# Kernel optimization log

Measured on AMD Instinct MI355X. Metric: run time of the kernel, lower is better.

The kernel has to match this reference:

```python
import jax, jax.numpy as jnp
import numpy as np

H = 16            # num_heads
DK = 64           # head_k_dim = hidden*0.5/H
DV = 128          # head_v_dim = hidden*1.0/H
EPS = 1e-5
GATE_NORM = 16.0


def setup_inputs() -> dict:
    key = jax.random.key(0)
    ks = jax.random.split(key, 8)
    B, T, D = 4, 4096, 2048
    hidden_states = jax.random.normal(ks[0], (B, T, D), jnp.float32)
    state = jax.random.normal(ks[1], (B, H, DK, DV), jnp.float32)
    norm_w = jnp.ones((D,), jnp.float32)
    # fan-in scaled init so activations stay O(1)
    k_w = jax.random.normal(ks[2], (H * DK, D), jnp.float32) / np.sqrt(D)
    v_w = jax.random.normal(ks[3], (H * DV, D), jnp.float32) / np.sqrt(D)
    gk_w1 = jax.random.normal(ks[4], (16, D), jnp.float32) / np.sqrt(D)
    gk_w2 = jax.random.normal(ks[5], (H * DK, 16), jnp.float32) / np.sqrt(16)
    gk_b = jnp.zeros((H * DK,), jnp.float32)
    return {"hidden_states": hidden_states, "state": state, "norm_w": norm_w,
            "k_w": k_w, "v_w": v_w, "gk_w1": gk_w1, "gk_w2": gk_w2, "gk_b": gk_b}


def reference(hidden_states, state, norm_w, k_w, v_w, gk_w1, gk_w2, gk_b):
    B, T, D = hidden_states.shape
    # RMSNorm
    x = hidden_states * jax.lax.rsqrt(jnp.mean(hidden_states * hidden_states, -1, keepdims=True) + EPS)
    x = x * norm_w
    # projections -> [B,T,H,d]
    k = (x @ k_w.T).reshape(B, T, H, DK)
    v = (x @ v_w.T).reshape(B, T, H, DV)
    gk = jax.nn.log_sigmoid((x @ gk_w1.T) @ gk_w2.T + gk_b) / GATE_NORM  # <= 0
    gk = gk.reshape(B, T, H, DK)
    # GLA recurrence S_t = diag(exp(gk_t)) S_{t-1} + k_t^T v_t, unrolled:
    # S_T = exp(G_T) * S_0 + sum_t exp(G_T - G_t) * k_t v_t^T, G_t = cumsum(gk)
    G = jnp.cumsum(gk, axis=1)                       # [B,T,H,DK]
    g_total = G[:, -1]                               # [B,H,DK]
    decay = jnp.exp(G[:, -1:, :, :] - G)             # in (0,1], stable
    new_state = jnp.exp(g_total)[..., None] * state + \
        jnp.einsum('bthk,bthv->bhkv', k * decay, v)
    return new_state
```

## Files before the change

### kernel.cpp

```cpp
#include <hip/hip_runtime.h>

#define B_ 4
#define T_ 4096
#define D_ 2048
#define H_ 16
#define DK_ 64
#define DV_ 128
#define HDK 1024
#define HDV 2048
#define NN 3072
#define MM 16384
#define NT_ 32

typedef unsigned short u16;
typedef unsigned int u32;
typedef __attribute__((ext_vector_type(8))) short bf16x8;
typedef __attribute__((ext_vector_type(4))) float f32x4;

typedef const __attribute__((address_space(1))) u16 gu16;
typedef __attribute__((address_space(3))) u16 lu16;

__device__ __forceinline__ float b2f(u16 u) {
  u32 x = ((u32)u) << 16; float f; __builtin_memcpy(&f, &x, 4); return f;
}
__device__ __forceinline__ u16 f2b(float f) {
  u32 x; __builtin_memcpy(&x, &f, 4);
  u32 r = x + 0x7FFFu + ((x >> 16) & 1u);
  return (u16)(r >> 16);
}
__device__ __forceinline__ float fexp(float x) { return exp2f(x * 1.44269504f); }
__device__ __forceinline__ float flogsig(float z) {
  float u = exp2f(-fabsf(z) * 1.44269504f);
  float l = log2f(1.f + u) * 0.69314718f;
  return fminf(z, 0.f) - l;
}

__global__ __launch_bounds__(256) void k_cvtw(const float* __restrict__ kw,
                                              const float* __restrict__ vw,
                                              u16* __restrict__ Wb) {
  int i = blockIdx.x * 256 + threadIdx.x;
  size_t e = (size_t)i * 8;
  const float* src = (e < (size_t)HDK * D_) ? (kw + e) : (vw + (e - (size_t)HDK * D_));
  float4 f0 = ((const float4*)src)[0];
  float4 f1 = ((const float4*)src)[1];
  union { int4 v; u16 u[8]; } o;
  o.u[0] = f2b(f0.x); o.u[1] = f2b(f0.y); o.u[2] = f2b(f0.z); o.u[3] = f2b(f0.w);
  o.u[4] = f2b(f1.x); o.u[5] = f2b(f1.y); o.u[6] = f2b(f1.z); o.u[7] = f2b(f1.w);
  *(int4*)(Wb + e) = o.v;
}

__global__ __launch_bounds__(256) void k_rms(const float* __restrict__ hs,
                                             const float* __restrict__ nw,
                                             const float* __restrict__ w1,
                                             u16* __restrict__ xb,
                                             float* __restrict__ y) {
  int r0 = blockIdx.x * 4;
  int tid = threadIdx.x;
  int wv = tid >> 6, ln = tid & 63;
  __shared__ float red[4][4];
  __shared__ float ys[4][4][16];
  float x[4][8];
  float ssq[4];
  #pragma unroll
  for (int r = 0; r < 4; ++r) {
    const float4* hp = (const float4*)(hs + (size_t)(r0 + r) * D_);
    float4 a = hp[tid * 2], b = hp[tid * 2 + 1];
    x[r][0] = a.x; x[r][1] = a.y; x[r][2] = a.z; x[r][3] = a.w;
    x[r][4] = b.x; x[r][5] = b.y; x[r][6] = b.z; x[r][7] = b.w;
    float s = 0.f;
    #pragma unroll
    for (int i = 0; i < 8; ++i) s += x[r][i] * x[r][i];
    #pragma unroll
    for (int o = 32; o > 0; o >>= 1) s += __shfl_xor(s, o, 64);
    ssq[r] = s;
  }
  if (ln == 0) {
    #pragma unroll
    for (int r = 0; r < 4; ++r) red[wv][r] = ssq[r];
  }
  __syncthreads();
  const float4* np_ = (const float4*)nw;
  float4 n0 = np_[tid * 2], n1 = np_[tid * 2 + 1];
  float nwv[8] = {n0.x, n0.y, n0.z, n0.w, n1.x, n1.y, n1.z, n1.w};
  #pragma unroll
  for (int r = 0; r < 4; ++r) {
    float tot = red[0][r] + red[1][r] + red[2][r] + red[3][r];
    float inv = rsqrtf(tot * (1.f / D_) + 1e-5f);
    union { int4 v; u16 u[8]; } o;
    #pragma unroll
    for (int i = 0; i < 8; ++i) { x[r][i] = x[r][i] * inv * nwv[i]; o.u[i] = f2b(x[r][i]); }
    *(int4*)(xb + (size_t)(r0 + r) * D_ + tid * 8) = o.v;
  }
  float p[4][16];
  #pragma unroll
  for (int r = 0; r < 4; ++r)
    #pragma unroll
    for (int j = 0; j < 16; ++j) p[r][j] = 0.f;
  #pragma unroll
  for (int j = 0; j < 16; ++j) {
    const float4* wp = (const float4*)(w1 + (size_t)j * D_);
    float4 a = wp[tid * 2], b = wp[tid * 2 + 1];
    float wj[8] = {a.x, a.y, a.z, a.w, b.x, b.y, b.z, b.w};
    #pragma unroll
    for (int r = 0; r < 4; ++r) {
      float s = 0.f;
      #pragma unroll
      for (int i = 0; i < 8; ++i) s += x[r][i] * wj[i];
      p[r][j] = s;
    }
  }
  #pragma unroll
  for (int r = 0; r < 4; ++r)
    #pragma unroll
    for (int j = 0; j < 16; ++j) {
      float s = p[r][j];
      #pragma unroll
      for (int o = 32; o > 0; o >>= 1) s += __shfl_xor(s, o, 64);
      p[r][j] = s;
    }
  if (ln == 0) {
    for (int r = 0; r < 4; ++r)
      for (int j = 0; j < 16; ++j) ys[wv][r][j] = p[r][j];
  }
  __syncthreads();
  if (tid < 64) {
    int r = tid >> 4, j = tid & 15;
    y[(size_t)(r0 + r) * 16 + j] = ys[0][r][j] + ys[1][r][j] + ys[2][r][j] + ys[3][r][j];
  }
}

#define GLDS(SRC, DST) __builtin_amdgcn_global_load_lds((gu16*)(SRC), (lu16*)(DST), 16, 0, 0)

#define MFMA16(AF, MB) do {                                                    \
    __builtin_amdgcn_s_setprio(1);                                             \
    _Pragma("unroll")                                                          \
    for (int mi_ = 0; mi_ < 4; ++mi_)                                          \
      _Pragma("unroll")                                                        \
      for (int ni_ = 0; ni_ < 4; ++ni_)                                        \
        acc[(MB) + mi_][ni_] = __builtin_amdgcn_mfma_f32_16x16x32_bf16(        \
            AF[mi_], bf[ni_], acc[(MB) + mi_][ni_], 0, 0, 0);                  \
    __builtin_amdgcn_s_setprio(0);                                             \
    __builtin_amdgcn_sched_barrier(0);                                         \
  } while (0)

#define KTILE(DB, NB, VM0, VM2, ST) do {                                       \
           \
    asm volatile("s_waitcnt vmcnt(" VM0 ")" ::: "memory");                     \
    __builtin_amdgcn_s_barrier();                                              \
    __builtin_amdgcn_sched_barrier(0);                                         \
    _Pragma("unroll")                                                          \
    for (int mi_ = 0; mi_ < 4; ++mi_)                                          \
      af[mi_] = *(const bf16x8*)&SA[DB][0][(wr * 128 + mi_ * 16 + r) * 32 + kcol]; \
    _Pragma("unroll")                                                          \
    for (int ni_ = 0; ni_ < 4; ++ni_)                                          \
      bf[ni_] = *(const bf16x8*)&SB[DB][0][(wc * 64 + ni_ * 16 + r) * 32 + kcol]; \
    if (ST) { GLDS(An, &SA[NB][0][lw]); GLDS(An + 16 * D_, &SA[NB][0][lw + 512]); } \
    asm volatile("s_waitcnt lgkmcnt(0)" ::: "memory");                         \
    __builtin_amdgcn_sched_barrier(0);                                         \
    MFMA16(af, 0);                                                             \
                  \
    _Pragma("unroll")                                                          \
    for (int mi_ = 0; mi_ < 4; ++mi_)                                          \
      af2[mi_] = *(const bf16x8*)&SA[DB][0][(wr * 128 + (4 + mi_) * 16 + r) * 32 + kcol]; \
    if (ST) { GLDS(An + 32, &SA[NB][1][lw]); GLDS(An + 32 + 16 * D_, &SA[NB][1][lw + 512]); } \
    asm volatile("s_waitcnt lgkmcnt(0)" ::: "memory");                         \
    __builtin_amdgcn_sched_barrier(0);                                         \
    MFMA16(af2, 4);                                                            \
                       \
    asm volatile("s_waitcnt vmcnt(" VM2 ")" ::: "memory");                     \
    __builtin_amdgcn_s_barrier();                                              \
    __builtin_amdgcn_sched_barrier(0);                                         \
    _Pragma("unroll")                                                          \
    for (int mi_ = 0; mi_ < 4; ++mi_)                                          \
      af[mi_] = *(const bf16x8*)&SA[DB][1][(wr * 128 + mi_ * 16 + r) * 32 + kcol]; \
    _Pragma("unroll")                                                          \
    for (int ni_ = 0; ni_ < 4; ++ni_)                                          \
      bf[ni_] = *(const bf16x8*)&SB[DB][1][(wc * 64 + ni_ * 16 + r) * 32 + kcol]; \
    if (ST) { GLDS(Bn, &SB[NB][0][lw]); GLDS(Bn + 16 * D_, &SB[NB][0][lw + 512]); } \
    asm volatile("s_waitcnt lgkmcnt(0)" ::: "memory");                         \
    __builtin_amdgcn_sched_barrier(0);                                         \
    MFMA16(af, 0);                                                             \
                             \
    _Pragma("unroll")                                                          \
    for (int mi_ = 0; mi_ < 4; ++mi_)                                          \
      af2[mi_] = *(const bf16x8*)&SA[DB][1][(wr * 128 + (4 + mi_) * 16 + r) * 32 + kcol]; \
    if (ST) { GLDS(Bn + 32, &SB[NB][1][lw]); GLDS(Bn + 32 + 16 * D_, &SB[NB][1][lw + 512]); } \
    asm volatile("s_waitcnt lgkmcnt(0)" ::: "memory");                         \
    __builtin_amdgcn_sched_barrier(0);                                         \
    MFMA16(af2, 4);                                                            \
  } while (0)

__global__ __launch_bounds__(512, 2) void k_gemm(const u16* __restrict__ X,
                                                 const u16* __restrict__ W,
                                                 u16* __restrict__ C) {
  __shared__ u16 SA[2][2][8192];
  __shared__ u16 SB[2][2][8192];
  int bid = blockIdx.x;
  int swzb = (bid & 7) * 96 + (bid >> 3);
  int tm = swzb / 12, tn = swzb - tm * 12;
  int m0 = tm << 8, n0 = tn << 8;
  int tid = threadIdx.x;
  int w = tid >> 6, l = tid & 63;
  int wr = w >> 2, wc = w & 3;
  int arow = w * 32 + (l >> 2);
  int csw = 8 * ((l & 3) ^ ((l >> 3) & 3));
  const u16* Ag = X + (size_t)(m0 + arow) * D_ + csw;
  const u16* Bg = W + (size_t)(n0 + arow) * D_ + csw;
  int lw = w * 1024;
  int r = l & 15, kq = l >> 4;
  int kcol = 8 * (kq ^ ((r >> 1) & 3));

  f32x4 acc[8][4];
  #pragma unroll
  for (int mi = 0; mi < 8; ++mi)
    #pragma unroll
    for (int ni = 0; ni < 4; ++ni)
      #pragma unroll
      for (int q = 0; q < 4; ++q) acc[mi][ni][q] = 0.f;

  bf16x8 af[4], af2[4], bf[4];

  GLDS(Ag,           &SA[0][0][lw]);  GLDS(Ag + 16 * D_,      &SA[0][0][lw + 512]);
  GLDS(Ag + 32,      &SA[0][1][lw]);  GLDS(Ag + 32 + 16 * D_, &SA[0][1][lw + 512]);
  GLDS(Bg,           &SB[0][0][lw]);  GLDS(Bg + 16 * D_,      &SB[0][0][lw + 512]);
  GLDS(Bg + 32,      &SB[0][1][lw]);  GLDS(Bg + 32 + 16 * D_, &SB[0][1][lw + 512]);

  for (int kt = 0; kt < NT_ - 1; ++kt) {
    int db = kt & 1, nb = db ^ 1;
    const u16* An = Ag + (size_t)(kt + 1) * 64;
    const u16* Bn = Bg + (size_t)(kt + 1) * 64;
    KTILE(db, nb, "2", "4", 1);
  }
  {
    const u16* An = Ag;
    const u16* Bn = Bg;
    KTILE(1, 0, "2", "0", 0);
  }

  int cr = (l >> 4) * 4, cc = l & 15;
  #pragma unroll
  for (int mi = 0; mi < 8; ++mi)
    #pragma unroll
    for (int ni = 0; ni < 4; ++ni)
      #pragma unroll
      for (int q = 0; q < 4; ++q) {
        int gm = m0 + wr * 128 + mi * 16 + cr + q;
        int gn = n0 + wc * 64 + ni * 16 + cc;
        C[(size_t)gm * NN + gn] = f2b(acc[mi][ni][q]);
      }
}

__global__ __launch_bounds__(256) void k_gkcs(const float* __restrict__ y,
                                              const float* __restrict__ w2,
                                              const float* __restrict__ gb,
                                              u16* __restrict__ gkh,
                                              float* __restrict__ ct) {
  __shared__ float yl[64][16];
  int blk = blockIdx.x;
  int cg = blk & 3, tc = (blk >> 2) & 63, b = blk >> 8;
  int tid = threadIdx.x;
  int c = cg * 256 + tid;
  {
    int row = tid >> 2, q = tid & 3;
    const float4* src = (const float4*)(y + (size_t)(b * T_ + tc * 64 + row) * 16 + q * 4);
    *(float4*)&yl[row][q * 4] = *src;
  }
  float w2r[16];
  {
    const float4* wsrc = (const float4*)(w2 + (size_t)c * 16);
    float4 q0 = wsrc[0], q1 = wsrc[1], q2 = wsrc[2], q3 = wsrc[3];
    w2r[0] = q0.x; w2r[1] = q0.y; w2r[2] = q0.z; w2r[3] = q0.w;
    w2r[4] = q1.x; w2r[5] = q1.y; w2r[6] = q1.z; w2r[7] = q1.w;
    w2r[8] = q2.x; w2r[9] = q2.y; w2r[10] = q2.z; w2r[11] = q2.w;
    w2r[12] = q3.x; w2r[13] = q3.y; w2r[14] = q3.z; w2r[15] = q3.w;
  }
  float gbr = gb[c];
  __syncthreads();
  float sum = 0.f;
  size_t rowbase = (size_t)(b * T_ + tc * 64) * HDK + c;
  for (int t = 0; t < 64; ++t) {
    const float4* yv4 = (const float4*)&yl[t][0];
    float4 y0 = yv4[0], y1 = yv4[1], y2 = yv4[2], y3 = yv4[3];
    float z = gbr;
    z = fmaf(y0.x, w2r[0], z);  z = fmaf(y0.y, w2r[1], z);
    z = fmaf(y0.z, w2r[2], z);  z = fmaf(y0.w, w2r[3], z);
    z = fmaf(y1.x, w2r[4], z);  z = fmaf(y1.y, w2r[5], z);
    z = fmaf(y1.z, w2r[6], z);  z = fmaf(y1.w, w2r[7], z);
    z = fmaf(y2.x, w2r[8], z);  z = fmaf(y2.y, w2r[9], z);
    z = fmaf(y2.z, w2r[10], z); z = fmaf(y2.w, w2r[11], z);
    z = fmaf(y3.x, w2r[12], z); z = fmaf(y3.y, w2r[13], z);
    z = fmaf(y3.z, w2r[14], z); z = fmaf(y3.w, w2r[15], z);
    float g = flogsig(z) * (1.f / 16.f);
    _Float16 hv = (_Float16)g;
    u16 bits; __builtin_memcpy(&bits, &hv, 2);
    gkh[rowbase + (size_t)t * HDK] = bits;
    sum += (float)hv;
  }
  ct[(size_t)(b * 64 + tc) * HDK + c] = sum;
}

__global__ __launch_bounds__(256) void k_scan(const float* __restrict__ ct,
                                              float* __restrict__ co,
                                              float* __restrict__ gt) {
  int b = blockIdx.x >> 2, cg = blockIdx.x & 3;
  int c = cg * 256 + threadIdx.x;
  float run = 0.f;
  #pragma unroll 8
  for (int tc = 0; tc < 64; ++tc) {
    size_t idx = (size_t)(b * 64 + tc) * HDK + c;
    co[idx] = run;
    run += ct[idx];
  }
  gt[b * HDK + c] = run;
}

__global__ __launch_bounds__(256) void k_decay(const u16* __restrict__ gkh,
                                               const float* __restrict__ co,
                                               const float* __restrict__ gt,
                                               const u16* __restrict__ kv,
                                               u16* __restrict__ Ab) {
  int blk = blockIdx.x;
  int cg = blk & 3, tc = (blk >> 2) & 63, b = blk >> 8;
  int c = cg * 256 + threadIdx.x;
  float run = co[(size_t)(b * 64 + tc) * HDK + c];
  float g = gt[b * HDK + c];
  #pragma unroll 8
  for (int tt = 0; tt < 64; ++tt) {
    size_t row = (size_t)(b * T_) + tc * 64 + tt;
    u16 bits = gkh[row * HDK + c];
    _Float16 hv; __builtin_memcpy(&hv, &bits, 2);
    run += (float)hv;
    float decay = fexp(g - run);
    float kvl = b2f(kv[row * NN + c]);
    Ab[row * HDK + c] = f2b(kvl * decay);
  }
}

__global__ __launch_bounds__(256) void k_outer(const u16* __restrict__ Ab,
                                               const u16* __restrict__ kv,
                                               float* __restrict__ part) {
  __shared__ u16 At[2][64][40];
  __shared__ u16 Vt[2][128][40];
  int s = blockIdx.x, h = blockIdx.y, b = blockIdx.z;
  int tid = threadIdx.x;
  int w = tid >> 6, l = tid & 63;
  int adk = tid & 63, atq = tid >> 6;
  int vdv = tid & 127, vth = tid >> 7;
  int r = l & 15, q = l >> 4;
  f32x4 acc[8];
  #pragma unroll
  for (int n = 0; n < 8; ++n)
    #pragma unroll
    for (int j = 0; j < 4; ++j) acc[n][j] = 0.f;

  union { int4 v[2]; u16 u[16]; } vbuf;
  union { int4 v; u16 u[8]; } abuf;

  #define LOADT(KK) do {                                                              \
      int t0_ = s * 512 + (KK) * 32;                                                  \
      _Pragma("unroll")                                                               \
      for (int i = 0; i < 8; ++i)                                                     \
        abuf.u[i] = Ab[(size_t)(b * T_ + t0_ + atq * 8 + i) * HDK + h * DK_ + adk];   \
      _Pragma("unroll")                                                               \
      for (int i = 0; i < 16; ++i)                                                    \
        vbuf.u[i] = kv[(size_t)(b * T_ + t0_ + vth * 16 + i) * NN + HDK + h * DV_ + vdv]; \
    } while (0)

  #define WRITET(BF) do {                                                             \
      *(int4*)&At[BF][adk][atq * 8] = abuf.v;                                         \
      *(int4*)&Vt[BF][vdv][vth * 16] = vbuf.v[0];                                     \
      *(int4*)&Vt[BF][vdv][vth * 16 + 8] = vbuf.v[1];                                 \
    } while (0)

  LOADT(0);
  WRITET(0);
  for (int kk = 0; kk < 16; ++kk) {
    int cur = kk & 1;
    if (kk < 15) LOADT(kk + 1);
    __syncthreads();
    bf16x8 af = *(const bf16x8*)&At[cur][w * 16 + r][q * 8];
    #pragma unroll
    for (int n = 0; n < 8; ++n) {
      bf16x8 vf = *(const bf16x8*)&Vt[cur][n * 16 + r][q * 8];
      acc[n] = __builtin_amdgcn_mfma_f32_16x16x32_bf16(af, vf, acc[n], 0, 0, 0);
    }
    __syncthreads();
    if (kk < 15) WRITET(1 - cur);
  }
  #undef LOADT
  #undef WRITET

  float* dst = part + ((size_t)(b * H_ + h) * 8 + s) * (DK_ * DV_);
  #pragma unroll
  for (int n = 0; n < 8; ++n)
    #pragma unroll
    for (int j = 0; j < 4; ++j)
      dst[(w * 16 + q * 4 + j) * DV_ + n * 16 + r] = acc[n][j];
}

__global__ __launch_bounds__(256) void k_final(const float* __restrict__ part,
                                               const float* __restrict__ gt,
                                               const float* __restrict__ st,
                                               float* __restrict__ out) {
  int i = blockIdx.x * 256 + threadIdx.x;
  int dv = i & 127, dk = (i >> 7) & 63, h = (i >> 13) & 15, b = i >> 17;
  size_t base = ((size_t)(b * H_ + h) * 8) * 8192 + dk * DV_ + dv;
  float s = 0.f;
  #pragma unroll
  for (int sp = 0; sp < 8; ++sp) s += part[base + (size_t)sp * 8192];
  float g = gt[b * HDK + h * DK_ + dk];
  out[i] = fexp(g) * st[i] + s;
}

extern "C" void kernel_launch(void* const* d_in, const int* in_sizes, int n_in,
                              void* d_out, int out_size, void* d_ws, size_t ws_size,
                              hipStream_t stream) {
  const float* hs = (const float*)d_in[0];
  const float* st = (const float*)d_in[1];
  const float* nw = (const float*)d_in[2];
  const float* kw = (const float*)d_in[3];
  const float* vw = (const float*)d_in[4];
  const float* w1 = (const float*)d_in[5];
  const float* w2 = (const float*)d_in[6];
  const float* gb = (const float*)d_in[7];
  float* out = (float*)d_out;
  char* ws = (char*)d_ws;

  u16*  Wb  = (u16*)(ws + 0);
  u16*  xb  = (u16*)(ws + 12582912);
  float* y  = (float*)(ws + 79691776);
  u16*  kv  = (u16*)(ws + 80740352);
  u16*  gkh = (u16*)(ws + 181403648);
  float* ct = (float*)(ws + 214958080);
  float* co = (float*)(ws + 216006656);
  float* gt = (float*)(ws + 217055232);
  u16*  Ab  = (u16*)(ws + 12582912);
  float* part = (float*)(ws + 12582912 + 33554432);

  k_cvtw<<<dim3(3072), dim3(256), 0, stream>>>(kw, vw, Wb);
  k_rms<<<dim3(4096), dim3(256), 0, stream>>>(hs, nw, w1, xb, y);
  k_gemm<<<dim3(768), dim3(512), 0, stream>>>(xb, Wb, kv);
  k_gkcs<<<dim3(1024), dim3(256), 0, stream>>>(y, w2, gb, gkh, ct);
  k_scan<<<dim3(16), dim3(256), 0, stream>>>(ct, co, gt);
  k_decay<<<dim3(1024), dim3(256), 0, stream>>>(gkh, co, gt, kv, Ab);
  k_outer<<<dim3(8, 16, 4), dim3(256), 0, stream>>>(Ab, kv, part);
  k_final<<<dim3(2048), dim3(256), 0, stream>>>(part, gt, st, out);
}
```

Before: 365.0 us.

## Load GEMM B operand directly from global into registers, bypassing LDS

```diff
diff --git a/kernel.cpp b/kernel.cpp
--- a/kernel.cpp
+++ b/kernel.cpp
@@ -131,70 +131,75 @@
 
 #define GLDS(SRC, DST) __builtin_amdgcn_global_load_lds((gu16*)(SRC), (lu16*)(DST), 16, 0, 0)
 
-#define MFMA16(AF, MB) do {                                                    \
+#define MFMA16B(AF, BB, MB) do {                                               \
     __builtin_amdgcn_s_setprio(1);                                             \
     _Pragma("unroll")                                                          \
     for (int mi_ = 0; mi_ < 4; ++mi_)                                          \
       _Pragma("unroll")                                                        \
       for (int ni_ = 0; ni_ < 4; ++ni_)                                        \
         acc[(MB) + mi_][ni_] = __builtin_amdgcn_mfma_f32_16x16x32_bf16(        \
-            AF[mi_], bf[ni_], acc[(MB) + mi_][ni_], 0, 0, 0);                  \
+            AF[mi_], BB[ni_], acc[(MB) + mi_][ni_], 0, 0, 0);                  \
     __builtin_amdgcn_s_setprio(0);                                             \
     __builtin_amdgcn_sched_barrier(0);                                         \
   } while (0)
 
-#define KTILE(DB, NB, VM0, VM2, ST) do {                                       \
-           \
+#define KTILEB(DB, NB, VM0, VM2, ST) do {                                      \
+                  \
     asm volatile("s_waitcnt vmcnt(" VM0 ")" ::: "memory");                     \
     __builtin_amdgcn_s_barrier();                                              \
     __builtin_amdgcn_sched_barrier(0);                                         \
     _Pragma("unroll")                                                          \
     for (int mi_ = 0; mi_ < 4; ++mi_)                                          \
       af[mi_] = *(const bf16x8*)&SA[DB][0][(wr * 128 + mi_ * 16 + r) * 32 + kcol]; \
-    _Pragma("unroll")                                                          \
-    for (int ni_ = 0; ni_ < 4; ++ni_)                                          \
-      bf[ni_] = *(const bf16x8*)&SB[DB][0][(wc * 64 + ni_ * 16 + r) * 32 + kcol]; \
     if (ST) { GLDS(An, &SA[NB][0][lw]); GLDS(An + 16 * D_, &SA[NB][0][lw + 512]); } \
+    __builtin_amdgcn_sched_barrier(0);                                         \
     asm volatile("s_waitcnt lgkmcnt(0)" ::: "memory");                         \
     __builtin_amdgcn_sched_barrier(0);                                         \
-    MFMA16(af, 0);                                                             \
-                  \
+    MFMA16B(af, b0, 0);                                                        \
+     \
     _Pragma("unroll")                                                          \
     for (int mi_ = 0; mi_ < 4; ++mi_)                                          \
       af2[mi_] = *(const bf16x8*)&SA[DB][0][(wr * 128 + (4 + mi_) * 16 + r) * 32 + kcol]; \
-    if (ST) { GLDS(An + 32, &SA[NB][1][lw]); GLDS(An + 32 + 16 * D_, &SA[NB][1][lw + 512]); } \
     asm volatile("s_waitcnt lgkmcnt(0)" ::: "memory");                         \
     __builtin_amdgcn_sched_barrier(0);                                         \
-    MFMA16(af2, 4);                                                            \
-                       \
+    MFMA16B(af2, b0, 4);                                                       \
+    if (ST) {                                                                  \
+      _Pragma("unroll")                                                        \
+      for (int ni_ = 0; ni_ < 4; ++ni_)                                        \
+        b0[ni_] = *(const bf16x8*)(Wn + (size_t)ni_ * 16 * D_);                \
+      __builtin_amdgcn_sched_barrier(0);                                       \
+    }                                                                          \
+                  \
     asm volatile("s_waitcnt vmcnt(" VM2 ")" ::: "memory");                     \
     __builtin_amdgcn_s_barrier();                                              \
     __builtin_amdgcn_sched_barrier(0);                                         \
     _Pragma("unroll")                                                          \
     for (int mi_ = 0; mi_ < 4; ++mi_)                                          \
       af[mi_] = *(const bf16x8*)&SA[DB][1][(wr * 128 + mi_ * 16 + r) * 32 + kcol]; \
-    _Pragma("unroll")                                                          \
-    for (int ni_ = 0; ni_ < 4; ++ni_)                                          \
-      bf[ni_] = *(const bf16x8*)&SB[DB][1][(wc * 64 + ni_ * 16 + r) * 32 + kcol]; \
-    if (ST) { GLDS(Bn, &SB[NB][0][lw]); GLDS(Bn + 16 * D_, &SB[NB][0][lw + 512]); } \
+    if (ST) { GLDS(An + 32, &SA[NB][1][lw]); GLDS(An + 32 + 16 * D_, &SA[NB][1][lw + 512]); } \
+    __builtin_amdgcn_sched_barrier(0);                                         \
     asm volatile("s_waitcnt lgkmcnt(0)" ::: "memory");                         \
     __builtin_amdgcn_sched_barrier(0);                                         \
-    MFMA16(af, 0);                                                             \
-                             \
+    MFMA16B(af, b1, 0);                                                        \
+     \
     _Pragma("unroll")                                                          \
     for (int mi_ = 0; mi_ < 4; ++mi_)                                          \
       af2[mi_] = *(const bf16x8*)&SA[DB][1][(wr * 128 + (4 + mi_) * 16 + r) * 32 + kcol]; \
-    if (ST) { GLDS(Bn + 32, &SB[NB][1][lw]); GLDS(Bn + 32 + 16 * D_, &SB[NB][1][lw + 512]); } \
     asm volatile("s_waitcnt lgkmcnt(0)" ::: "memory");                         \
     __builtin_amdgcn_sched_barrier(0);                                         \
-    MFMA16(af2, 4);                                                            \
+    MFMA16B(af2, b1, 4);                                                       \
+    if (ST) {                                                                  \
+      _Pragma("unroll")                                                        \
+      for (int ni_ = 0; ni_ < 4; ++ni_)                                        \
+        b1[ni_] = *(const bf16x8*)(Wn + (size_t)ni_ * 16 * D_ + 32);           \
+      __builtin_amdgcn_sched_barrier(0);                                       \
+    }                                                                          \
   } while (0)
 
 __global__ __launch_bounds__(512, 2) void k_gemm(const u16* __restrict__ X,
                                                  const u16* __restrict__ W,
                                                  u16* __restrict__ C) {
   __shared__ u16 SA[2][2][8192];
-  __shared__ u16 SB[2][2][8192];
   int bid = blockIdx.x;
   int swzb = (bid & 7) * 96 + (bid >> 3);
   int tm = swzb / 12, tn = swzb - tm * 12;
@@ -205,10 +210,10 @@
   int arow = w * 32 + (l >> 2);
   int csw = 8 * ((l & 3) ^ ((l >> 3) & 3));
   const u16* Ag = X + (size_t)(m0 + arow) * D_ + csw;
-  const u16* Bg = W + (size_t)(n0 + arow) * D_ + csw;
   int lw = w * 1024;
   int r = l & 15, kq = l >> 4;
   int kcol = 8 * (kq ^ ((r >> 1) & 3));
+  const u16* Wg = W + (size_t)(n0 + wc * 64 + r) * D_ + kq * 8;
 
   f32x4 acc[8][4];
   #pragma unroll
@@ -218,23 +223,31 @@
       #pragma unroll
       for (int q = 0; q < 4; ++q) acc[mi][ni][q] = 0.f;
 
-  bf16x8 af[4], af2[4], bf[4];
-
-  GLDS(Ag,           &SA[0][0][lw]);  GLDS(Ag + 16 * D_,      &SA[0][0][lw + 512]);
-  GLDS(Ag + 32,      &SA[0][1][lw]);  GLDS(Ag + 32 + 16 * D_, &SA[0][1][lw + 512]);
-  GLDS(Bg,           &SB[0][0][lw]);  GLDS(Bg + 16 * D_,      &SB[0][0][lw + 512]);
-  GLDS(Bg + 32,      &SB[0][1][lw]);  GLDS(Bg + 32 + 16 * D_, &SB[0][1][lw + 512]);
+  bf16x8 af[4], af2[4], b0[4], b1[4];
+
+  GLDS(Ag,      &SA[0][0][lw]);  GLDS(Ag + 16 * D_,      &SA[0][0][lw + 512]);
+  __builtin_amdgcn_sched_barrier(0);
+  #pragma unroll
+  for (int ni = 0; ni < 4; ++ni)
+    b0[ni] = *(const bf16x8*)(Wg + (size_t)ni * 16 * D_);
+  __builtin_amdgcn_sched_barrier(0);
+  GLDS(Ag + 32, &SA[0][1][lw]);  GLDS(Ag + 32 + 16 * D_, &SA[0][1][lw + 512]);
+  __builtin_amdgcn_sched_barrier(0);
+  #pragma unroll
+  for (int ni = 0; ni < 4; ++ni)
+    b1[ni] = *(const bf16x8*)(Wg + (size_t)ni * 16 * D_ + 32);
+  __builtin_amdgcn_sched_barrier(0);
 
   for (int kt = 0; kt < NT_ - 1; ++kt) {
     int db = kt & 1, nb = db ^ 1;
     const u16* An = Ag + (size_t)(kt + 1) * 64;
-    const u16* Bn = Bg + (size_t)(kt + 1) * 64;
-    KTILE(db, nb, "2", "4", 1);
+    const u16* Wn = Wg + (size_t)(kt + 1) * 64;
+    KTILEB(db, nb, "6", "6", 1);
   }
   {
     const u16* An = Ag;
-    const u16* Bn = Bg;
-    KTILE(1, 0, "2", "0", 0);
+    const u16* Wn = Wg;
+    KTILEB(1, 0, "6", "0", 0);
   }
 
   int cr = (l >> 4) * 4, cc = l & 15;
```

After: 433.9 us. +18.9%, slower.

## Fuse decay computation into outer-product kernel and drop intermediate Ab buffer

Applied to the files above, without the earlier changes.

```diff
diff --git a/kernel.cpp b/kernel.cpp
--- a/kernel.cpp
+++ b/kernel.cpp
@@ -144,7 +144,6 @@
   } while (0)
 
 #define KTILE(DB, NB, VM0, VM2, ST) do {                                       \
-           \
     asm volatile("s_waitcnt vmcnt(" VM0 ")" ::: "memory");                     \
     __builtin_amdgcn_s_barrier();                                              \
     __builtin_amdgcn_sched_barrier(0);                                         \
@@ -158,7 +157,6 @@
     asm volatile("s_waitcnt lgkmcnt(0)" ::: "memory");                         \
     __builtin_amdgcn_sched_barrier(0);                                         \
     MFMA16(af, 0);                                                             \
-                  \
     _Pragma("unroll")                                                          \
     for (int mi_ = 0; mi_ < 4; ++mi_)                                          \
       af2[mi_] = *(const bf16x8*)&SA[DB][0][(wr * 128 + (4 + mi_) * 16 + r) * 32 + kcol]; \
@@ -166,7 +164,6 @@
     asm volatile("s_waitcnt lgkmcnt(0)" ::: "memory");                         \
     __builtin_amdgcn_sched_barrier(0);                                         \
     MFMA16(af2, 4);                                                            \
-                       \
     asm volatile("s_waitcnt vmcnt(" VM2 ")" ::: "memory");                     \
     __builtin_amdgcn_s_barrier();                                              \
     __builtin_amdgcn_sched_barrier(0);                                         \
@@ -180,7 +177,6 @@
     asm volatile("s_waitcnt lgkmcnt(0)" ::: "memory");                         \
     __builtin_amdgcn_sched_barrier(0);                                         \
     MFMA16(af, 0);                                                             \
-                             \
     _Pragma("unroll")                                                          \
     for (int mi_ = 0; mi_ < 4; ++mi_)                                          \
       af2[mi_] = *(const bf16x8*)&SA[DB][1][(wr * 128 + (4 + mi_) * 16 + r) * 32 + kcol]; \
@@ -314,39 +310,22 @@
   gt[b * HDK + c] = run;
 }
 
-__global__ __launch_bounds__(256) void k_decay(const u16* __restrict__ gkh,
+__global__ __launch_bounds__(256) void k_outer(const u16* __restrict__ gkh,
+                                               const u16* __restrict__ kv,
                                                const float* __restrict__ co,
                                                const float* __restrict__ gt,
-                                               const u16* __restrict__ kv,
-                                               u16* __restrict__ Ab) {
-  int blk = blockIdx.x;
-  int cg = blk & 3, tc = (blk >> 2) & 63, b = blk >> 8;
-  int c = cg * 256 + threadIdx.x;
-  float run = co[(size_t)(b * 64 + tc) * HDK + c];
-  float g = gt[b * HDK + c];
-  #pragma unroll 8
-  for (int tt = 0; tt < 64; ++tt) {
-    size_t row = (size_t)(b * T_) + tc * 64 + tt;
-    u16 bits = gkh[row * HDK + c];
-    _Float16 hv; __builtin_memcpy(&hv, &bits, 2);
-    run += (float)hv;
-    float decay = fexp(g - run);
-    float kvl = b2f(kv[row * NN + c]);
-    Ab[row * HDK + c] = f2b(kvl * decay);
-  }
-}
-
-__global__ __launch_bounds__(256) void k_outer(const u16* __restrict__ Ab,
-                                               const u16* __restrict__ kv,
                                                float* __restrict__ part) {
   __shared__ u16 At[2][64][40];
   __shared__ u16 Vt[2][128][40];
+  __shared__ float s8lds[2][64][4];
   int s = blockIdx.x, h = blockIdx.y, b = blockIdx.z;
   int tid = threadIdx.x;
   int w = tid >> 6, l = tid & 63;
   int adk = tid & 63, atq = tid >> 6;
   int vdv = tid & 127, vth = tid >> 7;
   int r = l & 15, q = l >> 4;
+  int c = h * DK_ + adk;
+  float g = gt[b * HDK + c];
   f32x4 acc[8];
   #pragma unroll
   for (int n = 0; n < 8; ++n)
@@ -354,16 +333,51 @@
     for (int j = 0; j < 4; ++j) acc[n][j] = 0.f;
 
   union { int4 v[2]; u16 u[16]; } vbuf;
+  union { int4 v; u16 u[8]; } kbuf;
+  float gk8[8];
   union { int4 v; u16 u[8]; } abuf;
+  float cobuf = 0.f, tot_prev = 0.f;
 
   #define LOADT(KK) do {                                                              \
       int t0_ = s * 512 + (KK) * 32;                                                  \
       _Pragma("unroll")                                                               \
-      for (int i = 0; i < 8; ++i)                                                     \
-        abuf.u[i] = Ab[(size_t)(b * T_ + t0_ + atq * 8 + i) * HDK + h * DK_ + adk];   \
+      for (int i = 0; i < 8; ++i) {                                                   \
+        size_t row_ = (size_t)(b * T_ + t0_ + atq * 8 + i);                           \
+        u16 gb_ = gkh[row_ * HDK + c];                                                \
+        _Float16 hv_; __builtin_memcpy(&hv_, &gb_, 2);                                \
+        gk8[i] = (float)hv_;                                                          \
+        kbuf.u[i] = kv[row_ * NN + c];                                                \
+      }                                                                               \
       _Pragma("unroll")                                                               \
       for (int i = 0; i < 16; ++i)                                                    \
         vbuf.u[i] = kv[(size_t)(b * T_ + t0_ + vth * 16 + i) * NN + HDK + h * DV_ + vdv]; \
+      if (((KK) & 1) == 0)                                                            \
+        cobuf = co[(size_t)(b * 64 + s * 8 + ((KK) >> 1)) * HDK + c];                 \
+      float s8_ = ((gk8[0] + gk8[1]) + (gk8[2] + gk8[3]))                             \
+                + ((gk8[4] + gk8[5]) + (gk8[6] + gk8[7]));                            \
+      s8lds[(KK) & 1][adk][atq] = s8_;                                                \
+    } while (0)
+
+  #define DECAY(KK) do {                                                              \
+      float sv0 = s8lds[(KK) & 1][adk][0];                                            \
+      float sv1 = s8lds[(KK) & 1][adk][1];                                            \
+      float sv2 = s8lds[(KK) & 1][adk][2];                                            \
+      float sv3 = s8lds[(KK) & 1][adk][3];                                            \
+      float pre = (atq > 0 ? sv0 : 0.f) + (atq > 1 ? sv1 : 0.f) + (atq > 2 ? sv2 : 0.f); \
+      float base;                                                                     \
+      if (((KK) & 1) == 0) {                                                          \
+        base = cobuf;                                                                 \
+        tot_prev = base + ((sv0 + sv1) + (sv2 + sv3));                                \
+      } else {                                                                        \
+        base = tot_prev;                                                              \
+      }                                                                               \
+      float run_ = base + pre;                                                        \
+      _Pragma("unroll")                                                               \
+      for (int i = 0; i < 8; ++i) {                                                   \
+        run_ += gk8[i];                                                               \
+        float av_ = b2f(kbuf.u[i]) * fexp(g - run_);                                  \
+        abuf.u[i] = f2b(av_);                                                         \
+      }                                                                               \
     } while (0)
 
   #define WRITET(BF) do {                                                             \
@@ -373,6 +387,8 @@
     } while (0)
 
   LOADT(0);
+  __syncthreads();
+  DECAY(0);
   WRITET(0);
   for (int kk = 0; kk < 16; ++kk) {
     int cur = kk & 1;
@@ -384,10 +400,12 @@
       bf16x8 vf = *(const bf16x8*)&Vt[cur][n * 16 + r][q * 8];
       acc[n] = __builtin_amdgcn_mfma_f32_16x16x32_bf16(af, vf, acc[n], 0, 0, 0);
     }
+    if (kk < 15) DECAY(kk + 1);
     __syncthreads();
     if (kk < 15) WRITET(1 - cur);
   }
   #undef LOADT
+  #undef DECAY
   #undef WRITET
 
   float* dst = part + ((size_t)(b * H_ + h) * 8 + s) * (DK_ * DV_);
@@ -434,15 +452,13 @@
   float* ct = (float*)(ws + 214958080);
   float* co = (float*)(ws + 216006656);
   float* gt = (float*)(ws + 217055232);
-  u16*  Ab  = (u16*)(ws + 12582912);
-  float* part = (float*)(ws + 12582912 + 33554432);
+  float* part = (float*)(ws + 12582912);
 
   k_cvtw<<<dim3(3072), dim3(256), 0, stream>>>(kw, vw, Wb);
   k_rms<<<dim3(4096), dim3(256), 0, stream>>>(hs, nw, w1, xb, y);
   k_gemm<<<dim3(768), dim3(512), 0, stream>>>(xb, Wb, kv);
   k_gkcs<<<dim3(1024), dim3(256), 0, stream>>>(y, w2, gb, gkh, ct);
   k_scan<<<dim3(16), dim3(256), 0, stream>>>(ct, co, gt);
-  k_decay<<<dim3(1024), dim3(256), 0, stream>>>(gkh, co, gt, kv, Ab);
-  k_outer<<<dim3(8, 16, 4), dim3(256), 0, stream>>>(Ab, kv, part);
+  k_outer<<<dim3(8, 16, 4), dim3(256), 0, stream>>>(gkh, kv, co, gt, part);
   k_final<<<dim3(2048), dim3(256), 0, stream>>>(part, gt, st, out);
 }
```

After: 354.2 us. 3.0% less time.
